# Optimization experiments

Measured on AMD Instinct MI355X. Metric: run time of the kernel, lower is better.

The kernel has to match this reference:

```python
import jax, jax.numpy as jnp
import numpy as np

B, S, IN_DIM, EMBED, HEADS, WINDOW = 2, 2048, 1024, 1024, 16, 256
HEAD_DIM = EMBED // HEADS
NEG_FILL = -9.0e15


def setup_inputs() -> dict:
    key = jax.random.key(0)
    k1, k2, k3, k4 = jax.random.split(key, 4)
    x = jax.random.normal(k1, (B, S, IN_DIM), dtype=jnp.float32)
    # padding_mask: positions with value 1 get zeroed in q/k/v (matches masked_fill semantics)
    padding_mask = jax.random.randint(k2, (B, S), 0, 2, dtype=jnp.int32)
    # xavier-uniform-like init scale for the linear weights
    lim_qkv = np.sqrt(6.0 / (IN_DIM + 3 * EMBED)).astype(np.float32)
    lim_o = np.sqrt(6.0 / (EMBED + EMBED)).astype(np.float32)
    Wqkv = jax.random.uniform(k3, (3 * EMBED, IN_DIM), jnp.float32, -lim_qkv, lim_qkv)
    bqkv = jnp.zeros((3 * EMBED,), jnp.float32)
    Wo = jax.random.uniform(k4, (EMBED, EMBED), jnp.float32, -lim_o, lim_o)
    bo = jnp.zeros((EMBED,), jnp.float32)
    return {"x": x, "padding_mask": padding_mask, "Wqkv": Wqkv, "bqkv": bqkv, "Wo": Wo, "bo": bo}


def reference(x, padding_mask, Wqkv, bqkv, Wo, bo):
    b, s, _ = x.shape
    h, hd, pad = HEADS, HEAD_DIM, WINDOW // 2
    # qkv projection: torch Linear is x @ W.T + b
    qkv = x @ Wqkv.T + bqkv                      # [B, S, 3E]
    qkv = qkv.reshape(b, s, h, 3 * hd).transpose(0, 2, 1, 3)  # [B, H, S, 3*hd]
    q, k, v = jnp.split(qkv, 3, axis=-1)          # each [B, H, S, hd]
    # zero out padded positions in q, k, v where padding_mask == 1
    pm = (padding_mask != 0)[:, None, :, None]    # [B, 1, S, 1]
    q = jnp.where(pm, 0.0, q)
    k = jnp.where(pm, 0.0, k)
    v = jnp.where(pm, 0.0, v)
    # dense banded scores: identical math to the unfold-based band compute
    scores = jnp.einsum("bhsd,bhtd->bhst", q, k)  # [B, H, S, S]
    idx = jnp.arange(s)
    band = jnp.abs(idx[None, :] - idx[:, None]) <= pad  # |i-j| <= window/2
    scores = jnp.where(band, scores, jnp.float32(NEG_FILL))
    scores = scores / jnp.sqrt(jnp.float32(hd))   # original scales AFTER the fill
    attn = jax.nn.softmax(scores, axis=-1)        # [B, H, S, S]
    vals = jnp.einsum("bhst,bhtd->bhsd", attn, v)  # [B, H, S, hd]
    vals = vals.transpose(0, 2, 1, 3).reshape(b, s, h * hd)  # [B, S, E]
    return vals @ Wo.T + bo
```

## Files before the change

kernel.cpp:

```cpp
#include <hip/hip_runtime.h>
#include <stdint.h>

#define S_LEN 2048
#define EMBED 1024
#define HEADS 16
#define HD 64
#define M_ROWS 4096
#define N_QKV 3072
#define KDIM 1024
#define SP 2336
#define CLP 136

typedef __attribute__((ext_vector_type(8))) short short8;
typedef __attribute__((ext_vector_type(4))) float f32x4;

__device__ __forceinline__ unsigned short f2bf(float f) {
  union { float f; uint32_t u; } c; c.f = f;
  uint32_t u = c.u;
  u += 0x7fffu + ((u >> 16) & 1u);
  return (unsigned short)(u >> 16);
}

__device__ __forceinline__ void gload_lds16(const unsigned short* g, unsigned short* l) {
  __builtin_amdgcn_global_load_lds(
      (const __attribute__((address_space(1))) void*)g,
      (__attribute__((address_space(3))) void*)l, 16, 0, 0);
}

#define XQ 1048576
#define WQKVQ 786432
#define WOQ 262144
#define CVTQ (XQ + WQKVQ + WOQ)
#define HALOQ 147456
__global__ __launch_bounds__(256) void cvt3_kernel(
    const float* __restrict__ x, const float* __restrict__ wqkv, const float* __restrict__ wo,
    unsigned short* __restrict__ xb, unsigned short* __restrict__ wqkvb, unsigned short* __restrict__ wob,
    unsigned short* __restrict__ vTp) {
  int i = blockIdx.x * blockDim.x + threadIdx.x;
  if (i < CVTQ) {
    const float* s; unsigned short* d; int off;
    if (i < XQ)               { s = x;    d = xb;    off = i; }
    else if (i < XQ + WQKVQ)  { s = wqkv; d = wqkvb; off = i - XQ; }
    else                      { s = wo;   d = wob;   off = i - XQ - WQKVQ; }
    float4 f = reinterpret_cast<const float4*>(s)[off];
    ushort4 o;
    o.x = f2bf(f.x); o.y = f2bf(f.y); o.z = f2bf(f.z); o.w = f2bf(f.w);
    reinterpret_cast<ushort4*>(d)[off] = o;
  } else {
    int j = i - CVTQ;
    int row = j / 72, p = j % 72;
    int off = row * 584 + (p < 32 ? p : 544 + (p - 32));
    reinterpret_cast<ushort4*>(vTp)[off] = (ushort4){0, 0, 0, 0};
  }
}

__global__ __launch_bounds__(256) void gemm_qkv(
    const unsigned short* __restrict__ A, const unsigned short* __restrict__ Bm,
    const float* __restrict__ bias, const int* __restrict__ pm,
    unsigned short* __restrict__ qo, unsigned short* __restrict__ ko,
    unsigned short* __restrict__ vTp)
{
  __shared__ __align__(16) unsigned short smem[128 * CLP];
  unsigned short* As = smem;
  unsigned short* Bs = smem + 8192;
  const int t = threadIdx.x, wave = t >> 6, lane = t & 63;
  const int m16 = lane & 15, q4 = lane >> 4;
  const int wm = wave >> 1, wn = wave & 1;
  const int flat = blockIdx.y * 24 + blockIdx.x;
  const int xcd = flat & 7, bi = flat >> 3;
  const int mb = (xcd & 3) * 8 + (bi & 7);
  const int nb = (xcd >> 2) * 12 + (bi >> 3);
  const int srow = lane >> 2, scol = (lane & 3) << 3;
  const unsigned short* pA0 = A + (size_t)(mb * 128 + (wave * 2 + 0) * 16 + srow) * KDIM + scol;
  const unsigned short* pA1 = A + (size_t)(mb * 128 + (wave * 2 + 1) * 16 + srow) * KDIM + scol;
  const unsigned short* pB0 = Bm + (size_t)(nb * 128 + (wave * 2 + 0) * 16 + srow) * KDIM + scol;
  const unsigned short* pB1 = Bm + (size_t)(nb * 128 + (wave * 2 + 1) * 16 + srow) * KDIM + scol;
  f32x4 acc[4][4];
#pragma unroll
  for (int i_ = 0; i_ < 4; i_++)
#pragma unroll
    for (int j_ = 0; j_ < 4; j_++) acc[i_][j_] = (f32x4){0.f, 0.f, 0.f, 0.f};

  for (int kt = 0; kt < KDIM; kt += 64) {
    __syncthreads();
#pragma unroll
    for (int h = 0; h < 2; h++) {
      gload_lds16(pA0 + kt + h * 32, As + h * 4096 + (wave * 2 + 0) * 512);
      gload_lds16(pA1 + kt + h * 32, As + h * 4096 + (wave * 2 + 1) * 512);
      gload_lds16(pB0 + kt + h * 32, Bs + h * 4096 + (wave * 2 + 0) * 512);
      gload_lds16(pB1 + kt + h * 32, Bs + h * 4096 + (wave * 2 + 1) * 512);
    }
    __syncthreads();
#pragma unroll
    for (int h = 0; h < 2; h++) {
      short8 af[4], bf[4];
#pragma unroll
      for (int mt = 0; mt < 4; mt++)
        af[mt] = *reinterpret_cast<const short8*>(&As[h * 4096 + (wm * 64 + mt * 16 + m16) * 32 + q4 * 8]);
#pragma unroll
      for (int nt = 0; nt < 4; nt++)
        bf[nt] = *reinterpret_cast<const short8*>(&Bs[h * 4096 + (wn * 64 + nt * 16 + m16) * 32 + q4 * 8]);
#pragma unroll
      for (int mt = 0; mt < 4; mt++)
#pragma unroll
        for (int nt = 0; nt < 4; nt++)
          acc[mt][nt] = __builtin_amdgcn_mfma_f32_16x16x32_bf16(af[mt], bf[nt], acc[mt][nt], 0, 0, 0);
    }
  }

  __syncthreads();
  float pmv[4][4];
#pragma unroll
  for (int mt = 0; mt < 4; mt++)
#pragma unroll
    for (int reg = 0; reg < 4; reg++) {
      int row = mb * 128 + wm * 64 + mt * 16 + q4 * 4 + reg;
      pmv[mt][reg] = (pm[row] != 0) ? 0.0f : 1.0f;
    }
#pragma unroll
  for (int nt = 0; nt < 4; nt++) {
    int col = nb * 128 + wn * 64 + nt * 16 + m16;
    int cloc = wn * 64 + nt * 16 + m16;
    float bv = bias[col];
#pragma unroll
    for (int mt = 0; mt < 4; mt++) {
#pragma unroll
      for (int reg = 0; reg < 4; reg++) {
        int rloc = wm * 64 + mt * 16 + q4 * 4 + reg;
        smem[rloc * CLP + cloc] = f2bf((acc[mt][nt][reg] + bv) * pmv[mt][reg]);
      }
    }
  }
  __syncthreads();
  {
    int r = t >> 1, h2 = t & 1;
    int g0 = nb * 128 + h2 * 64;
    int rem = g0 % 192, h = g0 / 192;
    if (rem < 128) {
      int s = mb * 128 + r;
      unsigned short* base = (rem == 0) ? qo : ko;
      unsigned short* dst = base + ((size_t)(((s >> 11) * 16 + h) * 2048 + (s & 2047))) * 64;
      const unsigned short* srcl = &smem[r * CLP + h2 * 64];
#pragma unroll
      for (int j = 0; j < 8; j++)
        *reinterpret_cast<short8*>(dst + j * 8) = *reinterpret_cast<const short8*>(srcl + j * 8);
    }
  }
  {
    int nm3 = nb % 3;
    int vstart = (nm3 == 1) ? 0 : (nm3 == 2) ? 64 : -1;
    if (vstart >= 0) {
      int c64 = t & 63, qtr = t >> 6;
      int c = vstart + c64;
      int colg = nb * 128 + c, h = colg / 192, d = c64;
      int s0 = mb * 128;
      int bh = (s0 >> 11) * 16 + h;
      unsigned short* dst = vTp + (size_t)(bh * 64 + d) * SP + 128 + (s0 & 2047) + qtr * 32;
#pragma unroll
      for (int j8 = 0; j8 < 4; j8++) {
        short8 tmp;
#pragma unroll
        for (int jj = 0; jj < 8; jj++)
          tmp[jj] = (short)smem[(qtr * 32 + j8 * 8 + jj) * CLP + c];
        *reinterpret_cast<short8*>(dst + j8 * 8) = tmp;
      }
    }
  }
}

__global__ __launch_bounds__(256) void gemm_out(
    const unsigned short* __restrict__ A, const unsigned short* __restrict__ Bm,
    const float* __restrict__ bias, float* __restrict__ out)
{
  __shared__ __align__(16) unsigned char smemraw[64 * 132 * 4];
  unsigned short* As = (unsigned short*)smemraw;
  unsigned short* Bs = As + 4096;
  float* Cldf = (float*)smemraw;
  const int t = threadIdx.x, wave = t >> 6, lane = t & 63;
  const int m16 = lane & 15, q4 = lane >> 4;
  const int wm = wave >> 1, wn = wave & 1;
  const int flat = blockIdx.y * 8 + blockIdx.x;
  const int xcd = flat & 7, bi = flat >> 3;
  const int mb = xcd * 8 + (bi & 7);
  const int nb = bi >> 3;
  const int srow = lane >> 2, scol = (lane & 3) << 3;
  const unsigned short* pA  = A + (size_t)(mb * 64 + wave * 16 + srow) * KDIM + scol;
  const unsigned short* pB0 = Bm + (size_t)(nb * 128 + wave * 32 + srow) * KDIM + scol;
  const unsigned short* pB1 = Bm + (size_t)(nb * 128 + wave * 32 + 16 + srow) * KDIM + scol;
  f32x4 acc[2][4];
#pragma unroll
  for (int i_ = 0; i_ < 2; i_++)
#pragma unroll
    for (int j_ = 0; j_ < 4; j_++) acc[i_][j_] = (f32x4){0.f, 0.f, 0.f, 0.f};
  for (int kt = 0; kt < KDIM; kt += 64) {
    __syncthreads();
#pragma unroll
    for (int h = 0; h < 2; h++) {
      gload_lds16(pA + kt + h * 32,  As + h * 2048 + wave * 16 * 32);
      gload_lds16(pB0 + kt + h * 32, Bs + h * 4096 + (wave * 32) * 32);
      gload_lds16(pB1 + kt + h * 32, Bs + h * 4096 + (wave * 32 + 16) * 32);
    }
    __syncthreads();
#pragma unroll
    for (int h = 0; h < 2; h++) {
      short8 af[2], bf[4];
#pragma unroll
      for (int mt = 0; mt < 2; mt++)
        af[mt] = *reinterpret_cast<const short8*>(&As[h * 2048 + (wm * 32 + mt * 16 + m16) * 32 + q4 * 8]);
#pragma unroll
      for (int nt = 0; nt < 4; nt++)
        bf[nt] = *reinterpret_cast<const short8*>(&Bs[h * 4096 + (wn * 64 + nt * 16 + m16) * 32 + q4 * 8]);
#pragma unroll
      for (int mt = 0; mt < 2; mt++)
#pragma unroll
        for (int nt = 0; nt < 4; nt++)
          acc[mt][nt] = __builtin_amdgcn_mfma_f32_16x16x32_bf16(af[mt], bf[nt], acc[mt][nt], 0, 0, 0);
    }
  }
  __syncthreads();
#pragma unroll
  for (int nt = 0; nt < 4; nt++) {
    int col = nb * 128 + wn * 64 + nt * 16 + m16;
    int cloc = wn * 64 + nt * 16 + m16;
    float bv = bias[col];
#pragma unroll
    for (int mt = 0; mt < 2; mt++) {
#pragma unroll
      for (int reg = 0; reg < 4; reg++) {
        int rloc = wm * 32 + mt * 16 + q4 * 4 + reg;
        Cldf[rloc * 132 + cloc] = acc[mt][nt][reg] + bv;
      }
    }
  }
  __syncthreads();
  {
    int r = t >> 2, seg = t & 3;
    float* dst = out + (size_t)(mb * 64 + r) * EMBED + nb * 128 + seg * 32;
    const float* srcl = &Cldf[r * 132 + seg * 32];
#pragma unroll
    for (int j = 0; j < 8; j++)
      *reinterpret_cast<float4*>(dst + j * 4) = *reinterpret_cast<const float4*>(srcl + j * 4);
  }
}

__global__ __launch_bounds__(256, 4) void attn_kernel(
    const unsigned short* __restrict__ q, const unsigned short* __restrict__ k,
    const unsigned short* __restrict__ vTp, unsigned short* __restrict__ vals)
{
  __shared__ __align__(16) unsigned short Pld[4][16][296];
  const int bid = blockIdx.x;
  const int bh = bid & 31, qtg = bid >> 5;
  const int lane = threadIdx.x & 63, wave = threadIdx.x >> 6;
  const int qt = qtg * 4 + wave;
  const int i0 = qt * 16, w0 = i0 - 128;
  const int m16 = lane & 15, q4 = lane >> 4;

  const unsigned short* qb = q + ((size_t)(bh * 2048 + i0 + m16)) * 64 + q4 * 8;
  short8 aq0 = *reinterpret_cast<const short8*>(qb);
  short8 aq1 = *reinterpret_cast<const short8*>(qb + 32);

  float sum[4] = {0.f, 0.f, 0.f, 0.f};
#pragma unroll
  for (int ct = 0; ct < 18; ct++) {
    int js = w0 + ct * 16 + m16;
    int jc = js < 0 ? 0 : (js > 2047 ? 2047 : js);
    const unsigned short* kb = k + ((size_t)(bh * 2048 + jc)) * 64 + q4 * 8;
    short8 b0 = *reinterpret_cast<const short8*>(kb);
    short8 b1 = *reinterpret_cast<const short8*>(kb + 32);
    f32x4 a = {0.f, 0.f, 0.f, 0.f};
    a = __builtin_amdgcn_mfma_f32_16x16x32_bf16(aq0, b0, a, 0, 0, 0);
    a = __builtin_amdgcn_mfma_f32_16x16x32_bf16(aq1, b1, a, 0, 0, 0);
#pragma unroll
    for (int reg = 0; reg < 4; reg++) {
      int i = i0 + q4 * 4 + reg;
      bool valid = (js >= 0) && (js < 2048) && (js >= i - 128) && (js <= i + 128);
      float e = valid ? __expf(a[reg] * 0.125f) : 0.0f;
      sum[reg] += e;
      Pld[wave][q4 * 4 + reg][ct * 16 + m16] = f2bf(e);
    }
  }
  float rden[4];
#pragma unroll
  for (int reg = 0; reg < 4; reg++) {
    float s = sum[reg];
    s += __shfl_xor(s, 1);
    s += __shfl_xor(s, 2);
    s += __shfl_xor(s, 4);
    s += __shfl_xor(s, 8);
    rden[reg] = 1.0f / s;
  }
  __syncthreads();
  short8 ap[9];
#pragma unroll
  for (int kc = 0; kc < 9; kc++)
    ap[kc] = *reinterpret_cast<const short8*>(&Pld[wave][m16][kc * 32 + q4 * 8]);

  const int b = bh >> 4, h = bh & 15;
#pragma unroll
  for (int dt = 0; dt < 4; dt++) {
    f32x4 av = {0.f, 0.f, 0.f, 0.f};
    const unsigned short* vb = vTp + ((size_t)(bh * 64 + dt * 16 + m16)) * SP + i0 + q4 * 8;
#pragma unroll
    for (int kc = 0; kc < 9; kc++) {
      short8 bv = *reinterpret_cast<const short8*>(vb + kc * 32);
      av = __builtin_amdgcn_mfma_f32_16x16x32_bf16(ap[kc], bv, av, 0, 0, 0);
    }
#pragma unroll
    for (int reg = 0; reg < 4; reg++)
      Pld[wave][q4 * 4 + reg][dt * 16 + m16] = f2bf(av[reg] * rden[reg]);
  }
  {
    int srow = lane >> 2, seg = lane & 3;
    unsigned short* dst = vals + ((size_t)(b * 2048 + i0 + srow)) * 1024 + h * 64 + seg * 16;
    const unsigned short* srcl = &Pld[wave][srow][seg * 16];
    *reinterpret_cast<short8*>(dst)     = *reinterpret_cast<const short8*>(srcl);
    *reinterpret_cast<short8*>(dst + 8) = *reinterpret_cast<const short8*>(srcl + 8);
  }
}

extern "C" void kernel_launch(void* const* d_in, const int* in_sizes, int n_in,
                              void* d_out, int out_size, void* d_ws, size_t ws_size,
                              hipStream_t stream) {
  const float* x    = (const float*)d_in[0];
  const int*   pm   = (const int*)d_in[1];
  const float* Wqkv = (const float*)d_in[2];
  const float* bqkv = (const float*)d_in[3];
  const float* Wo   = (const float*)d_in[4];
  const float* bo   = (const float*)d_in[5];
  float* out = (float*)d_out;
  char* ws = (char*)d_ws;

  unsigned short* xb    = (unsigned short*)(ws);
  unsigned short* vals  = (unsigned short*)(ws);
  unsigned short* Wqkvb = (unsigned short*)(ws +  8388608);
  unsigned short* Wob   = (unsigned short*)(ws + 14680064);
  unsigned short* qbuf  = (unsigned short*)(ws + 16777216);
  unsigned short* kbuf  = (unsigned short*)(ws + 25165824);
  unsigned short* vTp   = (unsigned short*)(ws + 33554432);

  cvt3_kernel<<<8768, 256, 0, stream>>>(x, Wqkv, Wo, xb, Wqkvb, Wob, vTp);
  gemm_qkv<<<dim3(24, 32), 256, 0, stream>>>(xb, Wqkvb, bqkv, pm, qbuf, kbuf, vTp);
  attn_kernel<<<1024, 256, 0, stream>>>(qbuf, kbuf, vTp, vals);
  gemm_out<<<dim3(8, 64), 256, 0, stream>>>(vals, Wob, bo, out);
}
```

Measured before the change: 183.8 us.

## Shrink GEMM tiles for more blocks and skip dead attention column tiles

The QKV GEMM tile drops from 128x128 to 64x128 and the output GEMM tile from 64x128 to 64x64. This doubles the grid sizes so the 256 CUs see more blocks and LDS use per block goes down. The epilogues are rewritten to match, with waves 0-1 writing q/k and waves 2-3 writing the V transpose. The attention kernel now skips the QK^T MFMA and exp work for column tiles that lie wholly outside the sequence, plus the always-empty 18th tile, and writes zeros there instead. The smaller tiles give less operand reuse per block and more global and L2 traffic.

```diff
diff --git a/kernel.cpp b/kernel.cpp
--- a/kernel.cpp
+++ b/kernel.cpp
@@ -60,24 +60,23 @@
     unsigned short* __restrict__ qo, unsigned short* __restrict__ ko,
     unsigned short* __restrict__ vTp)
 {
-  __shared__ __align__(16) unsigned short smem[128 * CLP];
+  __shared__ __align__(16) unsigned short smem[12288];
   unsigned short* As = smem;
-  unsigned short* Bs = smem + 8192;
+  unsigned short* Bs = smem + 4096;
   const int t = threadIdx.x, wave = t >> 6, lane = t & 63;
   const int m16 = lane & 15, q4 = lane >> 4;
   const int wm = wave >> 1, wn = wave & 1;
   const int flat = blockIdx.y * 24 + blockIdx.x;
   const int xcd = flat & 7, bi = flat >> 3;
-  const int mb = (xcd & 3) * 8 + (bi & 7);
-  const int nb = (xcd >> 2) * 12 + (bi >> 3);
+  const int mb = (xcd & 3) * 16 + (bi & 15);
+  const int nb = (xcd >> 2) * 12 + (bi >> 4);
   const int srow = lane >> 2, scol = (lane & 3) << 3;
-  const unsigned short* pA0 = A + (size_t)(mb * 128 + (wave * 2 + 0) * 16 + srow) * KDIM + scol;
-  const unsigned short* pA1 = A + (size_t)(mb * 128 + (wave * 2 + 1) * 16 + srow) * KDIM + scol;
-  const unsigned short* pB0 = Bm + (size_t)(nb * 128 + (wave * 2 + 0) * 16 + srow) * KDIM + scol;
-  const unsigned short* pB1 = Bm + (size_t)(nb * 128 + (wave * 2 + 1) * 16 + srow) * KDIM + scol;
-  f32x4 acc[4][4];
-#pragma unroll
-  for (int i_ = 0; i_ < 4; i_++)
+  const unsigned short* pA  = A + (size_t)(mb * 64 + wave * 16 + srow) * KDIM + scol;
+  const unsigned short* pB0 = Bm + (size_t)(nb * 128 + wave * 32 + srow) * KDIM + scol;
+  const unsigned short* pB1 = Bm + (size_t)(nb * 128 + wave * 32 + 16 + srow) * KDIM + scol;
+  f32x4 acc[2][4];
+#pragma unroll
+  for (int i_ = 0; i_ < 2; i_++)
 #pragma unroll
     for (int j_ = 0; j_ < 4; j_++) acc[i_][j_] = (f32x4){0.f, 0.f, 0.f, 0.f};
 
@@ -85,23 +84,22 @@
     __syncthreads();
 #pragma unroll
     for (int h = 0; h < 2; h++) {
-      gload_lds16(pA0 + kt + h * 32, As + h * 4096 + (wave * 2 + 0) * 512);
-      gload_lds16(pA1 + kt + h * 32, As + h * 4096 + (wave * 2 + 1) * 512);
-      gload_lds16(pB0 + kt + h * 32, Bs + h * 4096 + (wave * 2 + 0) * 512);
-      gload_lds16(pB1 + kt + h * 32, Bs + h * 4096 + (wave * 2 + 1) * 512);
+      gload_lds16(pA + kt + h * 32,  As + h * 2048 + (wave * 16) * 32);
+      gload_lds16(pB0 + kt + h * 32, Bs + h * 4096 + (wave * 32) * 32);
+      gload_lds16(pB1 + kt + h * 32, Bs + h * 4096 + (wave * 32 + 16) * 32);
     }
     __syncthreads();
 #pragma unroll
     for (int h = 0; h < 2; h++) {
-      short8 af[4], bf[4];
-#pragma unroll
-      for (int mt = 0; mt < 4; mt++)
-        af[mt] = *reinterpret_cast<const short8*>(&As[h * 4096 + (wm * 64 + mt * 16 + m16) * 32 + q4 * 8]);
+      short8 af[2], bf[4];
+#pragma unroll
+      for (int mt = 0; mt < 2; mt++)
+        af[mt] = *reinterpret_cast<const short8*>(&As[h * 2048 + (wm * 32 + mt * 16 + m16) * 32 + q4 * 8]);
 #pragma unroll
       for (int nt = 0; nt < 4; nt++)
         bf[nt] = *reinterpret_cast<const short8*>(&Bs[h * 4096 + (wn * 64 + nt * 16 + m16) * 32 + q4 * 8]);
 #pragma unroll
-      for (int mt = 0; mt < 4; mt++)
+      for (int mt = 0; mt < 2; mt++)
 #pragma unroll
         for (int nt = 0; nt < 4; nt++)
           acc[mt][nt] = __builtin_amdgcn_mfma_f32_16x16x32_bf16(af[mt], bf[nt], acc[mt][nt], 0, 0, 0);
@@ -109,60 +107,59 @@
   }
 
   __syncthreads();
-  float pmv[4][4];
-#pragma unroll
-  for (int mt = 0; mt < 4; mt++)
+  float pmv[2][4];
+#pragma unroll
+  for (int mt = 0; mt < 2; mt++)
 #pragma unroll
     for (int reg = 0; reg < 4; reg++) {
-      int row = mb * 128 + wm * 64 + mt * 16 + q4 * 4 + reg;
+      int row = mb * 64 + wm * 32 + mt * 16 + q4 * 4 + reg;
       pmv[mt][reg] = (pm[row] != 0) ? 0.0f : 1.0f;
     }
 #pragma unroll
   for (int nt = 0; nt < 4; nt++) {
-    int col = nb * 128 + wn * 64 + nt * 16 + m16;
     int cloc = wn * 64 + nt * 16 + m16;
-    float bv = bias[col];
-#pragma unroll
-    for (int mt = 0; mt < 4; mt++) {
+    float bv = bias[nb * 128 + cloc];
+#pragma unroll
+    for (int mt = 0; mt < 2; mt++) {
 #pragma unroll
       for (int reg = 0; reg < 4; reg++) {
-        int rloc = wm * 64 + mt * 16 + q4 * 4 + reg;
+        int rloc = wm * 32 + mt * 16 + q4 * 4 + reg;
         smem[rloc * CLP + cloc] = f2bf((acc[mt][nt][reg] + bv) * pmv[mt][reg]);
       }
     }
   }
   __syncthreads();
   {
-    int r = t >> 1, h2 = t & 1;
-    int g0 = nb * 128 + h2 * 64;
-    int rem = g0 % 192, h = g0 / 192;
-    if (rem < 128) {
-      int s = mb * 128 + r;
-      unsigned short* base = (rem == 0) ? qo : ko;
-      unsigned short* dst = base + ((size_t)(((s >> 11) * 16 + h) * 2048 + (s & 2047))) * 64;
-      const unsigned short* srcl = &smem[r * CLP + h2 * 64];
-#pragma unroll
-      for (int j = 0; j < 8; j++)
-        *reinterpret_cast<short8*>(dst + j * 8) = *reinterpret_cast<const short8*>(srcl + j * 8);
-    }
-  }
-  {
-    int nm3 = nb % 3;
-    int vstart = (nm3 == 1) ? 0 : (nm3 == 2) ? 64 : -1;
-    if (vstart >= 0) {
-      int c64 = t & 63, qtr = t >> 6;
-      int c = vstart + c64;
-      int colg = nb * 128 + c, h = colg / 192, d = c64;
-      int s0 = mb * 128;
-      int bh = (s0 >> 11) * 16 + h;
-      unsigned short* dst = vTp + (size_t)(bh * 64 + d) * SP + 128 + (s0 & 2047) + qtr * 32;
-#pragma unroll
-      for (int j8 = 0; j8 < 4; j8++) {
-        short8 tmp;
-#pragma unroll
-        for (int jj = 0; jj < 8; jj++)
-          tmp[jj] = (short)smem[(qtr * 32 + j8 * 8 + jj) * CLP + c];
-        *reinterpret_cast<short8*>(dst + j8 * 8) = tmp;
+    int part = t >> 6, r = t & 63;
+    if (part < 2) {
+      int g0 = nb * 128 + part * 64;
+      int rem = g0 % 192, h = g0 / 192;
+      if (rem < 128) {
+        int s = mb * 64 + r;
+        unsigned short* base = (rem == 0) ? qo : ko;
+        unsigned short* dst = base + ((size_t)(((s >> 11) * 16 + h) * 2048 + (s & 2047))) * 64;
+        const unsigned short* srcl = &smem[r * CLP + part * 64];
+#pragma unroll
+        for (int j = 0; j < 8; j++)
+          *reinterpret_cast<short8*>(dst + j * 8) = *reinterpret_cast<const short8*>(srcl + j * 8);
+      }
+    } else {
+      int nm3 = nb % 3;
+      int vstart = (nm3 == 1) ? 0 : (nm3 == 2) ? 64 : -1;
+      if (vstart >= 0) {
+        int half = part - 2, c = vstart + r;
+        int colg = nb * 128 + c, h = colg / 192, d = r;
+        int s0 = mb * 64;
+        int bh = (s0 >> 11) * 16 + h;
+        unsigned short* dst = vTp + (size_t)(bh * 64 + d) * SP + 128 + (s0 & 2047) + half * 32;
+#pragma unroll
+        for (int j8 = 0; j8 < 4; j8++) {
+          short8 tmp;
+#pragma unroll
+          for (int jj = 0; jj < 8; jj++)
+            tmp[jj] = (short)smem[(half * 32 + j8 * 8 + jj) * CLP + c];
+          *reinterpret_cast<short8*>(dst + j8 * 8) = tmp;
+        }
       }
     }
   }
@@ -172,73 +169,70 @@
     const unsigned short* __restrict__ A, const unsigned short* __restrict__ Bm,
     const float* __restrict__ bias, float* __restrict__ out)
 {
-  __shared__ __align__(16) unsigned char smemraw[64 * 132 * 4];
+  __shared__ __align__(16) unsigned char smemraw[17408];
   unsigned short* As = (unsigned short*)smemraw;
   unsigned short* Bs = As + 4096;
   float* Cldf = (float*)smemraw;
   const int t = threadIdx.x, wave = t >> 6, lane = t & 63;
   const int m16 = lane & 15, q4 = lane >> 4;
   const int wm = wave >> 1, wn = wave & 1;
-  const int flat = blockIdx.y * 8 + blockIdx.x;
+  const int flat = blockIdx.y * 16 + blockIdx.x;
   const int xcd = flat & 7, bi = flat >> 3;
   const int mb = xcd * 8 + (bi & 7);
   const int nb = bi >> 3;
   const int srow = lane >> 2, scol = (lane & 3) << 3;
-  const unsigned short* pA  = A + (size_t)(mb * 64 + wave * 16 + srow) * KDIM + scol;
-  const unsigned short* pB0 = Bm + (size_t)(nb * 128 + wave * 32 + srow) * KDIM + scol;
-  const unsigned short* pB1 = Bm + (size_t)(nb * 128 + wave * 32 + 16 + srow) * KDIM + scol;
-  f32x4 acc[2][4];
+  const unsigned short* pA = A + (size_t)(mb * 64 + wave * 16 + srow) * KDIM + scol;
+  const unsigned short* pB = Bm + (size_t)(nb * 64 + wave * 16 + srow) * KDIM + scol;
+  f32x4 acc[2][2];
 #pragma unroll
   for (int i_ = 0; i_ < 2; i_++)
 #pragma unroll
-    for (int j_ = 0; j_ < 4; j_++) acc[i_][j_] = (f32x4){0.f, 0.f, 0.f, 0.f};
+    for (int j_ = 0; j_ < 2; j_++) acc[i_][j_] = (f32x4){0.f, 0.f, 0.f, 0.f};
   for (int kt = 0; kt < KDIM; kt += 64) {
     __syncthreads();
 #pragma unroll
     for (int h = 0; h < 2; h++) {
-      gload_lds16(pA + kt + h * 32,  As + h * 2048 + wave * 16 * 32);
-      gload_lds16(pB0 + kt + h * 32, Bs + h * 4096 + (wave * 32) * 32);
-      gload_lds16(pB1 + kt + h * 32, Bs + h * 4096 + (wave * 32 + 16) * 32);
+      gload_lds16(pA + kt + h * 32, As + h * 2048 + (wave * 16) * 32);
+      gload_lds16(pB + kt + h * 32, Bs + h * 2048 + (wave * 16) * 32);
     }
     __syncthreads();
 #pragma unroll
     for (int h = 0; h < 2; h++) {
-      short8 af[2], bf[4];
+      short8 af[2], bf[2];
 #pragma unroll
       for (int mt = 0; mt < 2; mt++)
         af[mt] = *reinterpret_cast<const short8*>(&As[h * 2048 + (wm * 32 + mt * 16 + m16) * 32 + q4 * 8]);
 #pragma unroll
-      for (int nt = 0; nt < 4; nt++)
-        bf[nt] = *reinterpret_cast<const short8*>(&Bs[h * 4096 + (wn * 64 + nt * 16 + m16) * 32 + q4 * 8]);
+      for (int nt = 0; nt < 2; nt++)
+        bf[nt] = *reinterpret_cast<const short8*>(&Bs[h * 2048 + (wn * 32 + nt * 16 + m16) * 32 + q4 * 8]);
 #pragma unroll
       for (int mt = 0; mt < 2; mt++)
 #pragma unroll
-        for (int nt = 0; nt < 4; nt++)
+        for (int nt = 0; nt < 2; nt++)
           acc[mt][nt] = __builtin_amdgcn_mfma_f32_16x16x32_bf16(af[mt], bf[nt], acc[mt][nt], 0, 0, 0);
     }
   }
   __syncthreads();
 #pragma unroll
-  for (int nt = 0; nt < 4; nt++) {
-    int col = nb * 128 + wn * 64 + nt * 16 + m16;
-    int cloc = wn * 64 + nt * 16 + m16;
-    float bv = bias[col];
+  for (int nt = 0; nt < 2; nt++) {
+    int cloc = wn * 32 + nt * 16 + m16;
+    float bv = bias[nb * 64 + cloc];
 #pragma unroll
     for (int mt = 0; mt < 2; mt++) {
 #pragma unroll
       for (int reg = 0; reg < 4; reg++) {
         int rloc = wm * 32 + mt * 16 + q4 * 4 + reg;
-        Cldf[rloc * 132 + cloc] = acc[mt][nt][reg] + bv;
+        Cldf[rloc * 68 + cloc] = acc[mt][nt][reg] + bv;
       }
     }
   }
   __syncthreads();
   {
     int r = t >> 2, seg = t & 3;
-    float* dst = out + (size_t)(mb * 64 + r) * EMBED + nb * 128 + seg * 32;
-    const float* srcl = &Cldf[r * 132 + seg * 32];
-#pragma unroll
-    for (int j = 0; j < 8; j++)
+    float* dst = out + (size_t)(mb * 64 + r) * EMBED + nb * 64 + seg * 16;
+    const float* srcl = &Cldf[r * 68 + seg * 16];
+#pragma unroll
+    for (int j = 0; j < 4; j++)
       *reinterpret_cast<float4*>(dst + j * 4) = *reinterpret_cast<const float4*>(srcl + j * 4);
   }
 }
@@ -262,21 +256,28 @@
   float sum[4] = {0.f, 0.f, 0.f, 0.f};
 #pragma unroll
   for (int ct = 0; ct < 18; ct++) {
-    int js = w0 + ct * 16 + m16;
-    int jc = js < 0 ? 0 : (js > 2047 ? 2047 : js);
-    const unsigned short* kb = k + ((size_t)(bh * 2048 + jc)) * 64 + q4 * 8;
-    short8 b0 = *reinterpret_cast<const short8*>(kb);
-    short8 b1 = *reinterpret_cast<const short8*>(kb + 32);
-    f32x4 a = {0.f, 0.f, 0.f, 0.f};
-    a = __builtin_amdgcn_mfma_f32_16x16x32_bf16(aq0, b0, a, 0, 0, 0);
-    a = __builtin_amdgcn_mfma_f32_16x16x32_bf16(aq1, b1, a, 0, 0, 0);
-#pragma unroll
-    for (int reg = 0; reg < 4; reg++) {
-      int i = i0 + q4 * 4 + reg;
-      bool valid = (js >= 0) && (js < 2048) && (js >= i - 128) && (js <= i + 128);
-      float e = valid ? __expf(a[reg] * 0.125f) : 0.0f;
-      sum[reg] += e;
-      Pld[wave][q4 * 4 + reg][ct * 16 + m16] = f2bf(e);
+    bool live = (ct < 17) && (w0 + ct * 16 + 15 >= 0) && (w0 + ct * 16 < 2048);
+    if (live) {
+      int js = w0 + ct * 16 + m16;
+      int jc = js < 0 ? 0 : (js > 2047 ? 2047 : js);
+      const unsigned short* kb = k + ((size_t)(bh * 2048 + jc)) * 64 + q4 * 8;
+      short8 b0 = *reinterpret_cast<const short8*>(kb);
+      short8 b1 = *reinterpret_cast<const short8*>(kb + 32);
+      f32x4 a = {0.f, 0.f, 0.f, 0.f};
+      a = __builtin_amdgcn_mfma_f32_16x16x32_bf16(aq0, b0, a, 0, 0, 0);
+      a = __builtin_amdgcn_mfma_f32_16x16x32_bf16(aq1, b1, a, 0, 0, 0);
+#pragma unroll
+      for (int reg = 0; reg < 4; reg++) {
+        int i = i0 + q4 * 4 + reg;
+        bool valid = (js >= 0) && (js < 2048) && (js >= i - 128) && (js <= i + 128);
+        float e = valid ? __expf(a[reg] * 0.125f) : 0.0f;
+        sum[reg] += e;
+        Pld[wave][q4 * 4 + reg][ct * 16 + m16] = f2bf(e);
+      }
+    } else {
+#pragma unroll
+      for (int reg = 0; reg < 4; reg++)
+        Pld[wave][q4 * 4 + reg][ct * 16 + m16] = 0;
     }
   }
   float rden[4];
@@ -339,7 +340,7 @@
   unsigned short* vTp   = (unsigned short*)(ws + 33554432);
 
   cvt3_kernel<<<8768, 256, 0, stream>>>(x, Wqkv, Wo, xb, Wqkvb, Wob, vTp);
-  gemm_qkv<<<dim3(24, 32), 256, 0, stream>>>(xb, Wqkvb, bqkv, pm, qbuf, kbuf, vTp);
+  gemm_qkv<<<dim3(24, 64), 256, 0, stream>>>(xb, Wqkvb, bqkv, pm, qbuf, kbuf, vTp);
   attn_kernel<<<1024, 256, 0, stream>>>(qbuf, kbuf, vTp, vals);
-  gemm_out<<<dim3(8, 64), 256, 0, stream>>>(vals, Wob, bo, out);
-}
+  gemm_out<<<dim3(16, 64), 256, 0, stream>>>(vals, Wob, bo, out);
+}
```

After: 179.5 us. -2.4%, faster.
